# Kernel tuning notes

Measured on AMD Instinct MI355X. Metric: run time of the kernel, lower is better.

## Reference

```python
import jax, jax.numpy as jnp
import numpy as np

N = 50000
E = 1600000
D_IN = 512
EPS = 1e-5


def setup_inputs() -> dict:
    key = jax.random.key(0)
    ks = jax.random.split(key, 20)
    p = lambda k, shape: jax.random.normal(k, shape, dtype=jnp.float32) * 0.05
    return {
        "x": jax.random.normal(ks[0], (N, D_IN), dtype=jnp.float32),
        "edge_index": jax.random.randint(ks[1], (2, E), 0, N),
        "edge_weight": jax.random.uniform(ks[2], (E,), dtype=jnp.float32),
        # conv1: ChebConv(512->400) with K=1,2,3 (weight per Chebyshev order)
        "W1a": p(ks[3], (1, D_IN, 400)), "b1a": p(ks[4], (400,)),
        "W1b": p(ks[5], (2, D_IN, 400)), "b1b": p(ks[6], (400,)),
        "W1c": p(ks[7], (3, D_IN, 400)), "b1c": p(ks[8], (400,)),
        "g1": jnp.ones((1200,), jnp.float32), "beta1": jnp.zeros((1200,), jnp.float32),
        # conv2: ChebConv(1200->100) with K=1,2,3
        "W2a": p(ks[9], (1, 1200, 100)), "b2a": p(ks[10], (100,)),
        "W2b": p(ks[11], (2, 1200, 100)), "b2b": p(ks[12], (100,)),
        "W2c": p(ks[13], (3, 1200, 100)), "b2c": p(ks[14], (100,)),
        "g2": jnp.ones((300,), jnp.float32), "beta2": jnp.zeros((300,), jnp.float32),
        "Wl": p(ks[15], (300, 10)), "bl": p(ks[16], (10,)),
    }


def _cheb(x, row, col, norm, W, b):
    """PyG ChebConv forward: out = sum_k T_k(L_hat) x @ W[k] + b.
    L_hat (sym norm, lambda_max=2) = -D^{-1/2} A D^{-1/2}, zero diagonal,
    applied as scatter: (L_hat h)[col] += norm_e * h[row]."""
    K = W.shape[0]
    n = x.shape[0]
    prop = lambda h: jax.ops.segment_sum(norm[:, None] * h[row], col, num_segments=n)
    out = x @ W[0]
    Tx_prev, Tx = x, None
    if K >= 2:
        Tx = prop(x)
        out = out + Tx @ W[1]
    for k in range(2, K):
        Tx_new = 2.0 * prop(Tx) - Tx_prev
        out = out + Tx_new @ W[k]
        Tx_prev, Tx = Tx, Tx_new
    return out + b


def _bn(h, g, beta):
    # BatchNorm over nodes (training-mode batch statistics, biased var)
    mu = h.mean(axis=0)
    var = h.var(axis=0)
    return (h - mu) * jax.lax.rsqrt(var + EPS) * g + beta


def reference(x, edge_index, edge_weight, W1a, b1a, W1b, b1b, W1c, b1c, g1, beta1,
              W2a, b2a, W2b, b2b, W2c, b2c, g2, beta2, Wl, bl):
    row, col = edge_index[0], edge_index[1]
    deg = jax.ops.segment_sum(edge_weight, row, num_segments=x.shape[0])
    safe = jnp.where(deg > 0, deg, 1.0)
    dis = jnp.where(deg > 0, jax.lax.rsqrt(safe), 0.0)  # deg^{-1/2}, inf -> 0
    norm = -dis[row] * edge_weight * dis[col]  # scaled-Laplacian edge weights

    h = jnp.concatenate([
        _cheb(x, row, col, norm, W1a, b1a),
        _cheb(x, row, col, norm, W1b, b1b),
        _cheb(x, row, col, norm, W1c, b1c)], axis=1)  # [N, 1200]
    h = jax.nn.relu(_bn(h, g1, beta1))

    h = jnp.concatenate([
        _cheb(h, row, col, norm, W2a, b2a),
        _cheb(h, row, col, norm, W2b, b2b),
        _cheb(h, row, col, norm, W2c, b2c)], axis=1)  # [N, 300]
    h = _bn(h, g2, beta2)

    logits = h @ Wl + bl  # [N, 10]
    return jax.nn.log_softmax(logits, axis=1)
```

## Files before the change

kernel.cpp:

```cpp
#include <hip/hip_runtime.h>
#include <math.h>

#define EPSB 1e-5f

typedef __attribute__((ext_vector_type(8))) short short8;
typedef __attribute__((ext_vector_type(4))) float floatx4;
typedef __attribute__((ext_vector_type(2))) float floatx2;

__device__ inline float bf2f(unsigned short h) {
  union { unsigned int u; float f; } v; v.u = ((unsigned int)h) << 16; return v.f;
}
__device__ inline unsigned short f2bf(float f) {
  union { float f; unsigned int u; } v; v.f = f;
  unsigned int r = v.u + 0x7fffu + ((v.u >> 16) & 1u);
  return (unsigned short)(r >> 16);
}

__device__ __forceinline__ void gl2lds16(const unsigned short* g, unsigned short* l) {
  __builtin_amdgcn_global_load_lds(
      (const __attribute__((address_space(1))) unsigned int*)g,
      (__attribute__((address_space(3))) unsigned int*)l, 16, 0, 0);
}

__device__ __forceinline__ void pk4(floatx2* a, uint4 g, floatx2 wv) {
  unsigned int u[4] = {g.x, g.y, g.z, g.w};
#pragma unroll
  for (int j = 0; j < 4; j++) {
    union { unsigned int q; float f; } lo, hi;
    lo.q = u[j] << 16;
    hi.q = u[j] & 0xffff0000u;
    floatx2 v; v[0] = lo.f; v[1] = hi.f;
    asm("v_pk_fma_f32 %0, %1, %2, %0" : "+v"(a[j]) : "v"(v), "v"(wv));
  }
}


__global__ void degcnt_kernel(const int* __restrict__ row, const int* __restrict__ col,
                              const float* __restrict__ ew,
                              float* __restrict__ deg, int* __restrict__ cnt, int E) {
  int e = blockIdx.x * blockDim.x + threadIdx.x;
  if (e < E) {
    atomicAdd(&deg[row[e]], ew[e]);
    atomicAdd(&cnt[col[e]], 1);
  }
}

__global__ void dis_kernel(float* deg, int n) {
  int i = blockIdx.x * blockDim.x + threadIdx.x;
  if (i < n) { float d = deg[i]; deg[i] = d > 0.f ? rsqrtf(d) : 0.f; }
}

__global__ __launch_bounds__(1024) void scan1_kernel(const int* __restrict__ cnt,
                                                     int* __restrict__ off,
                                                     int* __restrict__ bsum, int n) {
  __shared__ int buf[1024];
  int tid = threadIdx.x;
  int idx = blockIdx.x * 1024 + tid;
  int v = (idx < n) ? cnt[idx] : 0;
  buf[tid] = v;
  __syncthreads();
  for (int s = 1; s < 1024; s <<= 1) {
    int t = (tid >= s) ? buf[tid - s] : 0;
    __syncthreads();
    if (tid >= s) buf[tid] += t;
    __syncthreads();
  }
  if (idx < n) off[idx] = buf[tid] - v;
  if (tid == 1023) bsum[blockIdx.x] = buf[1023];
}

__global__ void scan2_kernel(int* __restrict__ bsum, int* __restrict__ off,
                             int nb, int n) {
  if (threadIdx.x == 0 && blockIdx.x == 0) {
    int run = 0;
    for (int k = 0; k < nb; k++) { int t = bsum[k]; bsum[k] = run; run += t; }
    off[n] = run;
  }
}

__global__ void scan3_kernel(int* __restrict__ off, const int* __restrict__ bsum, int n) {
  int i = blockIdx.x * blockDim.x + threadIdx.x;
  if (i < n) off[i] += bsum[i >> 10];
}

__global__ void copy_kernel(const int* __restrict__ src, int* __restrict__ dst, int n) {
  int i = blockIdx.x * blockDim.x + threadIdx.x;
  if (i < n) dst[i] = src[i];
}

__global__ void fill_kernel(const int* __restrict__ row, const int* __restrict__ col,
                            const float* __restrict__ ew, const float* __restrict__ dis,
                            int* __restrict__ wptr, int2* __restrict__ ePack, int E) {
  int e = blockIdx.x * blockDim.x + threadIdx.x;
  if (e < E) {
    int r = row[e], c = col[e];
    int p = atomicAdd(&wptr[c], 1);
    float nv = -dis[r] * ew[e] * dis[c];
    ePack[p] = make_int2(r, __float_as_int(nv));
  }
}


__global__ void cast_x_kernel(const float* __restrict__ x, unsigned short* __restrict__ xb,
                              int N) {
  int idx = blockIdx.x * blockDim.x + threadIdx.x;
  if (idx >= N * 128) return;
  int row = idx >> 7, c4 = idx & 127;
  float4 v = *reinterpret_cast<const float4*>(x + (size_t)row * 512 + c4 * 4);
  union { unsigned int u[2]; } p;
  p.u[0] = (unsigned int)f2bf(v.x) | ((unsigned int)f2bf(v.y) << 16);
  p.u[1] = (unsigned int)f2bf(v.z) | ((unsigned int)f2bf(v.w) << 16);
  *reinterpret_cast<uint2*>(xb + (size_t)row * 1536 + c4 * 4) = make_uint2(p.u[0], p.u[1]);
}

__global__ void wprep_kernel(const float* __restrict__ W, unsigned short* __restrict__ Bt,
                             int Ktot, int Nout, int ldBt, int rowOff) {
  int idx = blockIdx.x * blockDim.x + threadIdx.x;
  if (idx >= Ktot * Nout) return;
  int k = idx / Nout, n = idx - k * Nout;
  Bt[(size_t)(rowOff + n) * ldBt + k] = f2bf(W[idx]);
}

__global__ void padzero_kernel(unsigned short* __restrict__ h, int N) {
  int i = blockIdx.x * blockDim.x + threadIdx.x;
  if (i >= N * 2) return;
  *reinterpret_cast<uint4*>(h + (size_t)(i >> 1) * 1216 + 1200 + (i & 1) * 8) =
      make_uint4(0, 0, 0, 0);
}

__global__ void bcat_kernel(const float* __restrict__ a, const float* __restrict__ b,
                            const float* __restrict__ c, float* __restrict__ dst, int seg) {
  int i = blockIdx.x * blockDim.x + threadIdx.x;
  if (i >= 3 * seg) return;
  float v;
  if (i < seg) v = a[i];
  else if (i < 2 * seg) v = b[i - seg];
  else v = c[i - 2 * seg];
  dst[i] = v;
}

__global__ __launch_bounds__(256) void prop_chunk_kernel(
    unsigned short* __restrict__ base, int ld,
    int srcCol, int dstCol, int subCol,
    const int* __restrict__ off, const int2* __restrict__ ePack,
    float scale, int N) {
  int chunk = blockIdx.x & 7;
  int g = blockIdx.x >> 3;
  int tid = threadIdx.x;
  int slot = (tid >> 3) & 3;
  int c8 = tid & 7;
  int v = g * 8 + (tid >> 5);
  bool valid = v < N;
  int vv = valid ? v : N - 1;
  int co = chunk * 64 + c8 * 8;
  const unsigned short* src = base + srcCol + co;
  int s = off[vv], e = off[vv + 1];
  int len = e - s;
  int s0 = s + (len * slot >> 2);
  int e0 = s + (len * (slot + 1) >> 2);
  floatx2 a2[4] = {}, b2[4] = {};
  int i = s0;
  for (; i + 3 < e0; i += 4) {
    int2 p0 = ePack[i];
    int2 p1 = ePack[i + 1];
    int2 p2 = ePack[i + 2];
    int2 p3 = ePack[i + 3];
    uint4 g0 = *reinterpret_cast<const uint4*>(src + (size_t)p0.x * ld);
    uint4 g1 = *reinterpret_cast<const uint4*>(src + (size_t)p1.x * ld);
    uint4 g2 = *reinterpret_cast<const uint4*>(src + (size_t)p2.x * ld);
    uint4 g3 = *reinterpret_cast<const uint4*>(src + (size_t)p3.x * ld);
    floatx2 w0; w0[0] = w0[1] = __int_as_float(p0.y);
    floatx2 w1; w1[0] = w1[1] = __int_as_float(p1.y);
    floatx2 w2; w2[0] = w2[1] = __int_as_float(p2.y);
    floatx2 w3; w3[0] = w3[1] = __int_as_float(p3.y);
    pk4(a2, g0, w0);
    pk4(b2, g1, w1);
    pk4(a2, g2, w2);
    pk4(b2, g3, w3);
  }
  for (; i < e0; i++) {
    int2 p = ePack[i];
    uint4 gg = *reinterpret_cast<const uint4*>(src + (size_t)p.x * ld);
    floatx2 wv; wv[0] = wv[1] = __int_as_float(p.y);
    pk4(a2, gg, wv);
  }
  float a[8];
#pragma unroll
  for (int j = 0; j < 4; j++) {
    a[2 * j]     = a2[j][0] + b2[j][0];
    a[2 * j + 1] = a2[j][1] + b2[j][1];
  }
#pragma unroll
  for (int j = 0; j < 8; j++) {
    a[j] += __shfl_xor(a[j], 8);
    a[j] += __shfl_xor(a[j], 16);
  }
  if (slot != 0 || !valid) return;
  if (subCol >= 0) {
    uint4 sv = *reinterpret_cast<const uint4*>(base + subCol + co + (size_t)v * ld);
    a[0] = scale * a[0] - bf2f((unsigned short)(sv.x & 0xffff));
    a[1] = scale * a[1] - bf2f((unsigned short)(sv.x >> 16));
    a[2] = scale * a[2] - bf2f((unsigned short)(sv.y & 0xffff));
    a[3] = scale * a[3] - bf2f((unsigned short)(sv.y >> 16));
    a[4] = scale * a[4] - bf2f((unsigned short)(sv.z & 0xffff));
    a[5] = scale * a[5] - bf2f((unsigned short)(sv.z >> 16));
    a[6] = scale * a[6] - bf2f((unsigned short)(sv.w & 0xffff));
    a[7] = scale * a[7] - bf2f((unsigned short)(sv.w >> 16));
  }
  uint4 o;
  o.x = (unsigned int)f2bf(a[0]) | ((unsigned int)f2bf(a[1]) << 16);
  o.y = (unsigned int)f2bf(a[2]) | ((unsigned int)f2bf(a[3]) << 16);
  o.z = (unsigned int)f2bf(a[4]) | ((unsigned int)f2bf(a[5]) << 16);
  o.w = (unsigned int)f2bf(a[6]) | ((unsigned int)f2bf(a[7]) << 16);
  *reinterpret_cast<uint4*>(base + dstCol + co + (size_t)v * ld) = o;
}

__global__ void prop_z_kernel(const unsigned short* __restrict__ Zcat,
                              const int* __restrict__ off, const int2* __restrict__ ePack,
                              float* __restrict__ h2f, unsigned short* __restrict__ U1) {
  int v = blockIdx.x;
  int f8 = threadIdx.x;
  if (f8 >= 38) return;
  int s = off[v], e = off[v + 1];
  floatx2 a2[4] = {}, b2[4] = {};
  int i = s;
  for (; i + 3 < e; i += 4) {
    int2 p0 = ePack[i];
    int2 p1 = ePack[i + 1];
    int2 p2 = ePack[i + 2];
    int2 p3 = ePack[i + 3];
    uint4 g0 = *reinterpret_cast<const uint4*>(Zcat + (size_t)p0.x * 304 + f8 * 8);
    uint4 g1 = *reinterpret_cast<const uint4*>(Zcat + (size_t)p1.x * 304 + f8 * 8);
    uint4 g2 = *reinterpret_cast<const uint4*>(Zcat + (size_t)p2.x * 304 + f8 * 8);
    uint4 g3 = *reinterpret_cast<const uint4*>(Zcat + (size_t)p3.x * 304 + f8 * 8);
    floatx2 w0; w0[0] = w0[1] = __int_as_float(p0.y);
    floatx2 w1; w1[0] = w1[1] = __int_as_float(p1.y);
    floatx2 w2; w2[0] = w2[1] = __int_as_float(p2.y);
    floatx2 w3; w3[0] = w3[1] = __int_as_float(p3.y);
    pk4(a2, g0, w0);
    pk4(b2, g1, w1);
    pk4(a2, g2, w2);
    pk4(b2, g3, w3);
  }
  for (; i < e; i++) {
    int2 p = ePack[i];
    uint4 raw = *reinterpret_cast<const uint4*>(Zcat + (size_t)p.x * 304 + f8 * 8);
    floatx2 wv; wv[0] = wv[1] = __int_as_float(p.y);
    pk4(a2, raw, wv);
  }
  float a[8];
#pragma unroll
  for (int j = 0; j < 4; j++) {
    a[2 * j]     = a2[j][0] + b2[j][0];
    a[2 * j + 1] = a2[j][1] + b2[j][1];
  }
  if (f8 < 25) {
    float* p = h2f + (size_t)v * 300 + 100 + f8 * 8;
#pragma unroll
    for (int j = 0; j < 8; j++) p[j] += a[j];
  } else {
    uint4 o;
    o.x = (unsigned int)f2bf(a[0]) | ((unsigned int)f2bf(a[1]) << 16);
    o.y = (unsigned int)f2bf(a[2]) | ((unsigned int)f2bf(a[3]) << 16);
    o.z = (unsigned int)f2bf(a[4]) | ((unsigned int)f2bf(a[5]) << 16);
    o.w = (unsigned int)f2bf(a[6]) | ((unsigned int)f2bf(a[7]) << 16);
    *reinterpret_cast<uint4*>(U1 + (size_t)v * 104 + (f8 - 25) * 8) = o;
  }
}

__global__ void prop_u_kernel(const unsigned short* __restrict__ U1,
                              const int* __restrict__ off, const int2* __restrict__ ePack,
                              const unsigned short* __restrict__ Zcat,
                              float* __restrict__ h2f) {
  int v = blockIdx.x;
  int f8 = threadIdx.x;
  if (f8 >= 13) return;
  int s = off[v], e = off[v + 1];
  floatx2 a2[4] = {}, b2[4] = {};
  int i = s;
  for (; i + 3 < e; i += 4) {
    int2 p0 = ePack[i];
    int2 p1 = ePack[i + 1];
    int2 p2 = ePack[i + 2];
    int2 p3 = ePack[i + 3];
    uint4 g0 = *reinterpret_cast<const uint4*>(U1 + (size_t)p0.x * 104 + f8 * 8);
    uint4 g1 = *reinterpret_cast<const uint4*>(U1 + (size_t)p1.x * 104 + f8 * 8);
    uint4 g2 = *reinterpret_cast<const uint4*>(U1 + (size_t)p2.x * 104 + f8 * 8);
    uint4 g3 = *reinterpret_cast<const uint4*>(U1 + (size_t)p3.x * 104 + f8 * 8);
    floatx2 w0; w0[0] = w0[1] = __int_as_float(p0.y);
    floatx2 w1; w1[0] = w1[1] = __int_as_float(p1.y);
    floatx2 w2; w2[0] = w2[1] = __int_as_float(p2.y);
    floatx2 w3; w3[0] = w3[1] = __int_as_float(p3.y);
    pk4(a2, g0, w0);
    pk4(b2, g1, w1);
    pk4(a2, g2, w2);
    pk4(b2, g3, w3);
  }
  for (; i < e; i++) {
    int2 p = ePack[i];
    uint4 raw = *reinterpret_cast<const uint4*>(U1 + (size_t)p.x * 104 + f8 * 8);
    floatx2 wv; wv[0] = wv[1] = __int_as_float(p.y);
    pk4(a2, raw, wv);
  }
  float a[8];
#pragma unroll
  for (int j = 0; j < 4; j++) {
    a[2 * j]     = a2[j][0] + b2[j][0];
    a[2 * j + 1] = a2[j][1] + b2[j][1];
  }
  const unsigned short* z2 = Zcat + (size_t)v * 304 + 200;
  float* p = h2f + (size_t)v * 300 + 200;
#pragma unroll
  for (int j = 0; j < 8; j++) {
    int c = f8 * 8 + j;
    if (c < 100) p[c] += 2.f * a[j] - bf2f(z2[c]);
  }
}


__global__ __launch_bounds__(256) void gemm_l1_kernel(
    const unsigned short* __restrict__ A,
    const unsigned short* __restrict__ Bt,
    int M, const float* __restrict__ bias,
    unsigned short* __restrict__ Cb) {
  __shared__ __align__(16) unsigned short As[128 * 32];
  __shared__ __align__(16) unsigned short Bs[128 * 32];
  const int colTiles = 10;
  int rowTiles = (M + 127) >> 7;
  int L = blockIdx.x;
  int xcd = L & 7, slot = L >> 3;
  int rpx = (rowTiles + 7) >> 3;
  int rloc = slot / colTiles;
  int ct = slot - rloc * colTiles;
  int rt = xcd * rpx + rloc;
  if (rt >= rowTiles) return;
  int row0 = rt << 7, col0 = ct << 7;
  int Kt = (ct < 3) ? 512 : ((ct < 6) ? 1024 : 1536);

  int tid = threadIdx.x;
  int wave = tid >> 6, lane = tid & 63;
  int q = lane >> 4, mn = lane & 15;
  int wr = wave >> 1, wc = wave & 1;
  floatx4 acc[4][4] = {};

  const unsigned short* ga[2];
  const unsigned short* gb[2];
  unsigned short* la[2];
  unsigned short* lb[2];
#pragma unroll
  for (int j = 0; j < 2; j++) {
    int c = j * 256 + tid;
    int r = c >> 2, cw = (c & 3) * 8;
    int gr = row0 + r; if (gr > M - 1) gr = M - 1;
    ga[j] = A + (size_t)gr * 1536 + cw;
    gb[j] = Bt + (size_t)(col0 + r) * 1536 + cw;
    la[j] = &As[(j * 256 + wave * 64) * 8];
    lb[j] = &Bs[(j * 256 + wave * 64) * 8];
  }

  for (int k0 = 0; k0 < Kt; k0 += 32) {
#pragma unroll
    for (int j = 0; j < 2; j++) {
      gl2lds16(ga[j] + k0, la[j]);
      gl2lds16(gb[j] + k0, lb[j]);
    }
    __syncthreads();
    short8 af[4], bf[4];
#pragma unroll
    for (int i = 0; i < 4; i++) {
      af[i] = *reinterpret_cast<const short8*>(&As[(wr * 64 + i * 16 + mn) * 32 + q * 8]);
      bf[i] = *reinterpret_cast<const short8*>(&Bs[(wc * 64 + i * 16 + mn) * 32 + q * 8]);
    }
#pragma unroll
    for (int mi = 0; mi < 4; mi++)
#pragma unroll
      for (int ni = 0; ni < 4; ni++)
        acc[mi][ni] = __builtin_amdgcn_mfma_f32_16x16x32_bf16(af[mi], bf[ni], acc[mi][ni], 0, 0, 0);
    __syncthreads();
  }

#pragma unroll
  for (int mi = 0; mi < 4; mi++) {
#pragma unroll
    for (int ni = 0; ni < 4; ni++) {
      int gcol = col0 + wc * 64 + ni * 16 + mn;
      if (gcol >= 1200) continue;
      float b = bias[gcol];
#pragma unroll
      for (int r = 0; r < 4; r++) {
        int grow = row0 + wr * 64 + mi * 16 + q * 4 + r;
        if (grow >= M) continue;
        Cb[(size_t)grow * 1216 + gcol] = f2bf(acc[mi][ni][r] + b);
      }
    }
  }
}

__global__ __launch_bounds__(256) void gemm_l2_kernel(
    const unsigned short* __restrict__ A,
    const unsigned short* __restrict__ Bt,
    int M, const float* __restrict__ bias,
    unsigned short* __restrict__ Cb, float* __restrict__ Cf) {
  __shared__ __align__(16) unsigned short As[128 * 32];
  __shared__ __align__(16) unsigned short Bs[128 * 32];
  const int colTiles = 5;
  int rowTiles = (M + 127) >> 7;
  int L = blockIdx.x;
  int xcd = L & 7, slot = L >> 3;
  int rpx = (rowTiles + 7) >> 3;
  int rloc = slot / colTiles;
  int ct = slot - rloc * colTiles;
  int rt = xcd * rpx + rloc;
  if (rt >= rowTiles) return;
  int row0 = rt << 7, col0 = ct << 7;

  int tid = threadIdx.x;
  int wave = tid >> 6, lane = tid & 63;
  int q = lane >> 4, mn = lane & 15;
  int wr = wave >> 1, wc = wave & 1;
  floatx4 acc[4][4] = {};

  const unsigned short* ga[2];
  const unsigned short* gb[2];
  unsigned short* la[2];
  unsigned short* lb[2];
#pragma unroll
  for (int j = 0; j < 2; j++) {
    int c = j * 256 + tid;
    int r = c >> 2, cw = (c & 3) * 8;
    int gr = row0 + r; if (gr > M - 1) gr = M - 1;
    ga[j] = A + (size_t)gr * 1216 + cw;
    int gn = col0 + r; if (gn > 607) gn = 607;
    gb[j] = Bt + (size_t)gn * 1216 + cw;
    la[j] = &As[(j * 256 + wave * 64) * 8];
    lb[j] = &Bs[(j * 256 + wave * 64) * 8];
  }

  for (int k0 = 0; k0 < 1216; k0 += 32) {
#pragma unroll
    for (int j = 0; j < 2; j++) {
      gl2lds16(ga[j] + k0, la[j]);
      gl2lds16(gb[j] + k0, lb[j]);
    }
    __syncthreads();
    short8 af[4], bf[4];
#pragma unroll
    for (int i = 0; i < 4; i++) {
      af[i] = *reinterpret_cast<const short8*>(&As[(wr * 64 + i * 16 + mn) * 32 + q * 8]);
      bf[i] = *reinterpret_cast<const short8*>(&Bs[(wc * 64 + i * 16 + mn) * 32 + q * 8]);
    }
#pragma unroll
    for (int mi = 0; mi < 4; mi++)
#pragma unroll
      for (int ni = 0; ni < 4; ni++)
        acc[mi][ni] = __builtin_amdgcn_mfma_f32_16x16x32_bf16(af[mi], bf[ni], acc[mi][ni], 0, 0, 0);
    __syncthreads();
  }

#pragma unroll
  for (int mi = 0; mi < 4; mi++) {
#pragma unroll
    for (int ni = 0; ni < 4; ni++) {
      int gcol = col0 + wc * 64 + ni * 16 + mn;
      if (gcol < 300) {
        float b = bias[gcol];
#pragma unroll
        for (int r = 0; r < 4; r++) {
          int grow = row0 + wr * 64 + mi * 16 + q * 4 + r;
          if (grow >= M) continue;
          Cf[(size_t)grow * 300 + gcol] = acc[mi][ni][r] + b;
        }
      } else if (gcol >= 304 && gcol < 608) {
#pragma unroll
        for (int r = 0; r < 4; r++) {
          int grow = row0 + wr * 64 + mi * 16 + q * 4 + r;
          if (grow >= M) continue;
          Cb[(size_t)grow * 304 + (gcol - 304)] = f2bf(acc[mi][ni][r]);
        }
      }
    }
  }
}

__global__ void bn_stats_bf16_kernel(const unsigned short* __restrict__ h, int ld, int C,
                                     int N, float* __restrict__ sums) {
  int c = blockIdx.x * blockDim.x + threadIdx.x;
  if (c >= C) return;
  int r0 = blockIdx.y * 256;
  int r1 = min(N, r0 + 256);
  float s = 0.f, s2 = 0.f;
  for (int r = r0; r < r1; r++) {
    float v = bf2f(h[(size_t)r * ld + c]);
    s += v; s2 += v * v;
  }
  atomicAdd(&sums[c], s);
  atomicAdd(&sums[C + c], s2);
}

__global__ void scsh_kernel(const float* __restrict__ sums, const float* __restrict__ g,
                            const float* __restrict__ beta, float invN, int C,
                            float* __restrict__ scSh) {
  int c = blockIdx.x * blockDim.x + threadIdx.x;
  if (c >= C) return;
  float mu = sums[c] * invN;
  float var = sums[C + c] * invN - mu * mu;
  float s = rsqrtf(var + EPSB) * g[c];
  scSh[c] = s;
  scSh[C + c] = beta[c] - mu * s;
}

__global__ void bn_apply_bf16_kernel(unsigned short* __restrict__ h, int ld, int C8, int N,
                                     const float* __restrict__ scSh, int Cfull, int relu) {
  int idx = blockIdx.x * blockDim.x + threadIdx.x;
  if (idx >= N * C8) return;
  int row = idx / C8, c8 = idx - row * C8;
  unsigned short* p = h + (size_t)row * ld + c8 * 8;
  uint4 raw = *reinterpret_cast<uint4*>(p);
  float v[8];
  v[0] = bf2f((unsigned short)(raw.x & 0xffff)); v[1] = bf2f((unsigned short)(raw.x >> 16));
  v[2] = bf2f((unsigned short)(raw.y & 0xffff)); v[3] = bf2f((unsigned short)(raw.y >> 16));
  v[4] = bf2f((unsigned short)(raw.z & 0xffff)); v[5] = bf2f((unsigned short)(raw.z >> 16));
  v[6] = bf2f((unsigned short)(raw.w & 0xffff)); v[7] = bf2f((unsigned short)(raw.w >> 16));
#pragma unroll
  for (int j = 0; j < 8; j++) {
    int c = c8 * 8 + j;
    float o = v[j] * scSh[c] + scSh[Cfull + c];
    if (relu) o = fmaxf(o, 0.f);
    v[j] = o;
  }
  uint4 o;
  o.x = (unsigned int)f2bf(v[0]) | ((unsigned int)f2bf(v[1]) << 16);
  o.y = (unsigned int)f2bf(v[2]) | ((unsigned int)f2bf(v[3]) << 16);
  o.z = (unsigned int)f2bf(v[4]) | ((unsigned int)f2bf(v[5]) << 16);
  o.w = (unsigned int)f2bf(v[6]) | ((unsigned int)f2bf(v[7]) << 16);
  *reinterpret_cast<uint4*>(p) = o;
}

__global__ void bn_stats_kernel(const float* __restrict__ h, int C, int N,
                                float* __restrict__ sums) {
  int c = blockIdx.x * blockDim.x + threadIdx.x;
  if (c >= C) return;
  int r0 = blockIdx.y * 256;
  int r1 = min(N, r0 + 256);
  float s = 0.f, s2 = 0.f;
  for (int r = r0; r < r1; r++) {
    float v = h[(size_t)r * C + c];
    s += v; s2 += v * v;
  }
  atomicAdd(&sums[c], s);
  atomicAdd(&sums[C + c], s2);
}

__global__ void bn_apply_kernel(float* __restrict__ h, int C, int N,
                                const float* __restrict__ sums, const float* __restrict__ g,
                                const float* __restrict__ beta, float invN, int relu) {
  int C4 = C >> 2;
  int c4 = blockIdx.x * blockDim.x + threadIdx.x;
  if (c4 >= C4) return;
  float sc[4], sh[4];
#pragma unroll
  for (int j = 0; j < 4; j++) {
    int c = c4 * 4 + j;
    float mu = sums[c] * invN;
    float var = sums[C + c] * invN - mu * mu;
    float s = rsqrtf(var + EPSB) * g[c];
    sc[j] = s; sh[j] = beta[c] - mu * s;
  }
  int r0 = blockIdx.y * 256, r1 = min(N, r0 + 256);
  for (int r = r0; r < r1; r++) {
    float4* p = reinterpret_cast<float4*>(h + (size_t)r * C) + c4;
    float4 v = *p;
    v.x = v.x * sc[0] + sh[0]; v.y = v.y * sc[1] + sh[1];
    v.z = v.z * sc[2] + sh[2]; v.w = v.w * sc[3] + sh[3];
    if (relu) {
      v.x = fmaxf(v.x, 0.f); v.y = fmaxf(v.y, 0.f);
      v.z = fmaxf(v.z, 0.f); v.w = fmaxf(v.w, 0.f);
    }
    *p = v;
  }
}


__global__ __launch_bounds__(256) void final_bn_kernel(const float* __restrict__ h2,
                                                       const float* __restrict__ scSh,
                                                       const float* __restrict__ Wl,
                                                       const float* __restrict__ bl,
                                                       float* __restrict__ out, int N) {
  __shared__ float Ws[3000];
  __shared__ float S[600];
  for (int i = threadIdx.x; i < 3000; i += 256) Ws[i] = Wl[i];
  for (int i = threadIdx.x; i < 600; i += 256) S[i] = scSh[i];
  __syncthreads();
  int r = blockIdx.x * blockDim.x + threadIdx.x;
  if (r >= N) return;
  float acc[10];
#pragma unroll
  for (int c = 0; c < 10; c++) acc[c] = bl[c];
  const float* hr = h2 + (size_t)r * 300;
  for (int k = 0; k < 300; k++) {
    float x = hr[k] * S[k] + S[300 + k];
#pragma unroll
    for (int c = 0; c < 10; c++) acc[c] += x * Ws[k * 10 + c];
  }
  float mx = acc[0];
#pragma unroll
  for (int c = 1; c < 10; c++) mx = fmaxf(mx, acc[c]);
  float se = 0.f;
#pragma unroll
  for (int c = 0; c < 10; c++) se += expf(acc[c] - mx);
  float lz = mx + logf(se);
#pragma unroll
  for (int c = 0; c < 10; c++) out[(size_t)r * 10 + c] = acc[c] - lz;
}

__global__ __launch_bounds__(256) void final_kernel(const float* __restrict__ h2,
                                                    const float* __restrict__ Wl,
                                                    const float* __restrict__ bl,
                                                    float* __restrict__ out, int N) {
  __shared__ float Ws[3000];
  for (int i = threadIdx.x; i < 3000; i += 256) Ws[i] = Wl[i];
  __syncthreads();
  int r = blockIdx.x * blockDim.x + threadIdx.x;
  if (r >= N) return;
  float acc[10];
#pragma unroll
  for (int c = 0; c < 10; c++) acc[c] = bl[c];
  const float* hr = h2 + (size_t)r * 300;
  for (int k = 0; k < 300; k++) {
    float x = hr[k];
#pragma unroll
    for (int c = 0; c < 10; c++) acc[c] += x * Ws[k * 10 + c];
  }
  float mx = acc[0];
#pragma unroll
  for (int c = 1; c < 10; c++) mx = fmaxf(mx, acc[c]);
  float se = 0.f;
#pragma unroll
  for (int c = 0; c < 10; c++) se += expf(acc[c] - mx);
  float lz = mx + logf(se);
#pragma unroll
  for (int c = 0; c < 10; c++) out[(size_t)r * 10 + c] = acc[c] - lz;
}


__global__ void prop_kernel(const float* __restrict__ src, int srcLd4, int D4,
                            const int* __restrict__ off, const int2* __restrict__ ePack,
                            float* __restrict__ dst, int dstLd4,
                            const float* __restrict__ sub, int subLd4, float scale) {
  int v = blockIdx.x;
  int f4 = threadIdx.x;
  if (f4 >= D4) return;
  int s = off[v], e = off[v + 1];
  float ax = 0.f, ay = 0.f, az = 0.f, aw = 0.f;
  for (int i = s; i < e; i++) {
    int2 p = ePack[i];
    float w = __int_as_float(p.y);
    const float4 hv = *reinterpret_cast<const float4*>(src + ((size_t)p.x * srcLd4 + f4) * 4);
    ax += w * hv.x; ay += w * hv.y; az += w * hv.z; aw += w * hv.w;
  }
  float4 o;
  if (sub) {
    const float4 sv = *reinterpret_cast<const float4*>(sub + ((size_t)v * subLd4 + f4) * 4);
    o.x = scale * ax - sv.x; o.y = scale * ay - sv.y;
    o.z = scale * az - sv.z; o.w = scale * aw - sv.w;
  } else {
    o.x = ax; o.y = ay; o.z = az; o.w = aw;
  }
  *reinterpret_cast<float4*>(dst + ((size_t)v * dstLd4 + f4) * 4) = o;
}

#define BM 64
#define BN 64
#define BK 16

__global__ __launch_bounds__(256) void gemm_kernel(
    const float* __restrict__ A, int lda,
    const float* __restrict__ B, int ldb,
    float* __restrict__ C, int ldc, int c0,
    int M, int Nc, int K,
    const float* __restrict__ bias, int accumulate) {
  __shared__ float As[BK][BM + 4];
  __shared__ float Bs[BK][BN + 4];
  int tid = threadIdx.x;
  int tx = tid & 15, ty = tid >> 4;
  int row0 = blockIdx.y * BM, col0 = blockIdx.x * BN;
  float acc[4][4] = {};
  int aM = tid >> 2;
  int aK = (tid & 3) << 2;
  int bK = tid >> 4;
  int bN = (tid & 15) << 2;
  for (int k0 = 0; k0 < K; k0 += BK) {
    float4 av = make_float4(0.f, 0.f, 0.f, 0.f);
    int ar = row0 + aM;
    if (ar < M && k0 + aK < K)
      av = *reinterpret_cast<const float4*>(A + (size_t)ar * lda + k0 + aK);
    As[aK + 0][aM] = av.x; As[aK + 1][aM] = av.y;
    As[aK + 2][aM] = av.z; As[aK + 3][aM] = av.w;
    float4 bv = make_float4(0.f, 0.f, 0.f, 0.f);
    int bc = col0 + bN;
    if (bc < Nc && k0 + bK < K)
      bv = *reinterpret_cast<const float4*>(B + (size_t)(k0 + bK) * ldb + bc);
    Bs[bK][bN + 0] = bv.x; Bs[bK][bN + 1] = bv.y;
    Bs[bK][bN + 2] = bv.z; Bs[bK][bN + 3] = bv.w;
    __syncthreads();
#pragma unroll
    for (int k = 0; k < BK; k++) {
      float a0 = As[k][ty * 4 + 0], a1 = As[k][ty * 4 + 1];
      float a2 = As[k][ty * 4 + 2], a3 = As[k][ty * 4 + 3];
      float b0 = Bs[k][tx * 4 + 0], b1 = Bs[k][tx * 4 + 1];
      float b2 = Bs[k][tx * 4 + 2], b3 = Bs[k][tx * 4 + 3];
      acc[0][0] += a0 * b0; acc[0][1] += a0 * b1; acc[0][2] += a0 * b2; acc[0][3] += a0 * b3;
      acc[1][0] += a1 * b0; acc[1][1] += a1 * b1; acc[1][2] += a1 * b2; acc[1][3] += a1 * b3;
      acc[2][0] += a2 * b0; acc[2][1] += a2 * b1; acc[2][2] += a2 * b2; acc[2][3] += a2 * b3;
      acc[3][0] += a3 * b0; acc[3][1] += a3 * b1; acc[3][2] += a3 * b2; acc[3][3] += a3 * b3;
    }
    __syncthreads();
  }
#pragma unroll
  for (int i = 0; i < 4; i++) {
    int r = row0 + ty * 4 + i;
    if (r >= M) continue;
#pragma unroll
    for (int j = 0; j < 4; j++) {
      int c = col0 + tx * 4 + j;
      if (c >= Nc) continue;
      float v = acc[i][j];
      if (bias) v += bias[c];
      float* p = C + (size_t)r * ldc + c0 + c;
      if (accumulate) *p += v; else *p = v;
    }
  }
}


static inline int gemm_grid_ct(int M, int colTiles) {
  int rowTiles = (M + 127) >> 7;
  int rpx = (rowTiles + 7) >> 3;
  return 8 * rpx * colTiles;
}

extern "C" void kernel_launch(void* const* d_in, const int* in_sizes, int n_in,
                              void* d_out, int out_size, void* d_ws, size_t ws_size,
                              hipStream_t stream) {
  const float* x   = (const float*)d_in[0];
  const int*   ei  = (const int*)d_in[1];
  const float* ew  = (const float*)d_in[2];
  const float* W1a = (const float*)d_in[3];
  const float* b1a = (const float*)d_in[4];
  const float* W1b = (const float*)d_in[5];
  const float* b1b = (const float*)d_in[6];
  const float* W1c = (const float*)d_in[7];
  const float* b1c = (const float*)d_in[8];
  const float* g1  = (const float*)d_in[9];
  const float* be1 = (const float*)d_in[10];
  const float* W2a = (const float*)d_in[11];
  const float* b2a = (const float*)d_in[12];
  const float* W2b = (const float*)d_in[13];
  const float* b2b = (const float*)d_in[14];
  const float* W2c = (const float*)d_in[15];
  const float* b2c = (const float*)d_in[16];
  const float* g2  = (const float*)d_in[17];
  const float* be2 = (const float*)d_in[18];
  const float* Wl  = (const float*)d_in[19];
  const float* bl  = (const float*)d_in[20];
  float* out = (float*)d_out;

  const int N = in_sizes[0] / 512;
  const int E = in_sizes[1] / 2;
  const int* row = ei;
  const int* col = ei + E;
  (void)n_in; (void)out_size;

  int eb = (E + 255) / 256;
  int nb = (N + 255) / 256;
  int nb1 = (N + 1023) / 1024;

  char* ws = (char*)d_ws;
  size_t o = 0;
  int2*  ePack = (int2*)(ws + o);  o += (size_t)E * 8;
  float* dis   = (float*)(ws + o); o += (size_t)N * 4;
  int*   cnt   = (int*)(ws + o);   o += (size_t)N * 4;
  int*   off   = (int*)(ws + o);   o += (size_t)(N + 4) * 4;
  int*   wptr  = (int*)(ws + o);   o += (size_t)N * 4;
  int*   bsum  = (int*)(ws + o);   o += (size_t)(nb1 + 4) * 4;
  float* sums  = (float*)(ws + o); o += 2400 * 4;
  float* scSh  = (float*)(ws + o); o += 2400 * 4;
  float* bcat1 = (float*)(ws + o); o += 1200 * 4;
  float* bcat2 = (float*)(ws + o); o += 304 * 4;
  o = (o + 255) & ~(size_t)255;
  size_t oCommon = o;

  size_t oA = oCommon;
  unsigned short* BtL1 = (unsigned short*)(ws + oA); oA += (size_t)1280 * 1536 * 2;
  unsigned short* BtL2 = (unsigned short*)(ws + oA); oA += (size_t)640 * 1216 * 2;
  oA = (oA + 255) & ~(size_t)255;
  unsigned short* h1n = (unsigned short*)(ws + oA); oA += (size_t)N * 1216 * 2;
  oA = (oA + 255) & ~(size_t)255;
  float* h2f = (float*)(ws + oA); oA += (size_t)N * 300 * 4;
  oA = (oA + 255) & ~(size_t)255;
  unsigned short* Xcat = (unsigned short*)(ws + oA); oA += (size_t)N * 1536 * 2;
  unsigned short* Zcat = Xcat;
  unsigned short* U1 = Xcat + (size_t)N * 304;

  bool planA = (ws_size >= oA);

  hipMemsetAsync(dis, 0, (size_t)N * 4, stream);
  hipMemsetAsync(cnt, 0, (size_t)N * 4, stream);
  degcnt_kernel<<<eb, 256, 0, stream>>>(row, col, ew, dis, cnt, E);
  dis_kernel<<<nb, 256, 0, stream>>>(dis, N);
  scan1_kernel<<<nb1, 1024, 0, stream>>>(cnt, off, bsum, N);
  scan2_kernel<<<1, 64, 0, stream>>>(bsum, off, nb1, N);
  scan3_kernel<<<nb, 256, 0, stream>>>(off, bsum, N);
  copy_kernel<<<nb, 256, 0, stream>>>(off, wptr, N);
  fill_kernel<<<eb, 256, 0, stream>>>(row, col, ew, dis, wptr, ePack, E);

  if (planA) {
    hipMemsetAsync(BtL1, 0, (size_t)1280 * 1536 * 2, stream);
    hipMemsetAsync(BtL2, 0, (size_t)640 * 1216 * 2, stream);
    wprep_kernel<<<(400 * 512 + 255) / 256, 256, 0, stream>>>(W1a, BtL1, 512, 400, 1536, 0);
    wprep_kernel<<<(400 * 1024 + 255) / 256, 256, 0, stream>>>(W1b, BtL1, 1024, 400, 1536, 400);
    wprep_kernel<<<(400 * 1536 + 255) / 256, 256, 0, stream>>>(W1c, BtL1, 1536, 400, 1536, 800);
    wprep_kernel<<<(100 * 1200 + 255) / 256, 256, 0, stream>>>(W2a, BtL2, 1200, 100, 1216, 0);
    wprep_kernel<<<(100 * 1200 + 255) / 256, 256, 0, stream>>>(W2b, BtL2, 1200, 100, 1216, 100);
    wprep_kernel<<<(100 * 1200 + 255) / 256, 256, 0, stream>>>(W2c, BtL2, 1200, 100, 1216, 200);
    wprep_kernel<<<(100 * 1200 + 255) / 256, 256, 0, stream>>>(W2b + 1200 * 100, BtL2, 1200, 100, 1216, 304);
    wprep_kernel<<<(100 * 1200 + 255) / 256, 256, 0, stream>>>(W2c + 1200 * 100, BtL2, 1200, 100, 1216, 404);
    wprep_kernel<<<(100 * 1200 + 255) / 256, 256, 0, stream>>>(W2c + 2 * 1200 * 100, BtL2, 1200, 100, 1216, 504);
    bcat_kernel<<<(1200 + 255) / 256, 256, 0, stream>>>(b1a, b1b, b1c, bcat1, 400);
    bcat_kernel<<<(300 + 255) / 256, 256, 0, stream>>>(b2a, b2b, b2c, bcat2, 100);
    cast_x_kernel<<<(N * 128 + 255) / 256, 256, 0, stream>>>(x, Xcat, N);
    padzero_kernel<<<(N * 2 + 255) / 256, 256, 0, stream>>>(h1n, N);

    int gridP = ((N + 7) / 8) * 8;
    prop_chunk_kernel<<<gridP, 256, 0, stream>>>(Xcat, 1536, 0, 512, -1,
                                                 off, ePack, 1.f, N);
    prop_chunk_kernel<<<gridP, 256, 0, stream>>>(Xcat, 1536, 512, 1024, 0,
                                                 off, ePack, 2.f, N);

    gemm_l1_kernel<<<gemm_grid_ct(N, 10), 256, 0, stream>>>(Xcat, BtL1, N, bcat1, h1n);

    hipMemsetAsync(sums, 0, 2400 * 4, stream);
    dim3 s1g((1200 + 255) / 256, (N + 255) / 256);
    bn_stats_bf16_kernel<<<s1g, 256, 0, stream>>>(h1n, 1216, 1200, N, sums);
    scsh_kernel<<<(1200 + 255) / 256, 256, 0, stream>>>(sums, g1, be1, 1.f / (float)N, 1200, scSh);
    bn_apply_bf16_kernel<<<((size_t)N * 150 + 255) / 256, 256, 0, stream>>>(
        h1n, 1216, 150, N, scSh, 1200, 1);

    gemm_l2_kernel<<<gemm_grid_ct(N, 5), 256, 0, stream>>>(h1n, BtL2, N, bcat2, Zcat, h2f);

    prop_z_kernel<<<N, 64, 0, stream>>>(Zcat, off, ePack, h2f, U1);
    prop_u_kernel<<<N, 64, 0, stream>>>(U1, off, ePack, Zcat, h2f);

    hipMemsetAsync(sums, 0, 2400 * 4, stream);
    dim3 s2g((300 + 255) / 256, (N + 255) / 256);
    bn_stats_kernel<<<s2g, 256, 0, stream>>>(h2f, 300, N, sums);
    scsh_kernel<<<(300 + 255) / 256, 256, 0, stream>>>(sums, g2, be2, 1.f / (float)N, 300, scSh);
    final_bn_kernel<<<nb, 256, 0, stream>>>(h2f, scSh, Wl, bl, out, N);
    return;
  }

  size_t oB = oCommon;
  float* h2 = (float*)(ws + oB); oB += (size_t)N * 300 * 4;
  oB = (oB + 255) & ~(size_t)255;
  float* h1 = (float*)(ws + oB); oB += (size_t)N * 1200 * 4;
  oB = (oB + 255) & ~(size_t)255;
  size_t avail = (ws_size > oB) ? (ws_size - oB) : 0;
  int C1 = 64;
  { const int opts[4] = {512, 256, 128, 64};
    for (int i = 0; i < 4; i++)
      if ((size_t)2 * N * opts[i] * 4 <= avail) { C1 = opts[i]; break; } }
  int C2 = 100;
  { const int opts[6] = {1200, 600, 400, 300, 200, 100};
    for (int i = 0; i < 6; i++)
      if ((size_t)2 * N * opts[i] * 4 <= avail) { C2 = opts[i]; break; } }
  int maxC = C1 > C2 ? C1 : C2;
  float* S1 = (float*)(ws + oB);
  float* S2 = S1 + (size_t)N * maxC;

  dim3 g1d((400 + BN - 1) / BN, (N + BM - 1) / BM);
  gemm_kernel<<<g1d, 256, 0, stream>>>(x, 512, W1a, 400, h1, 1200, 0,   N, 400, 512, b1a, 0);
  gemm_kernel<<<g1d, 256, 0, stream>>>(x, 512, W1b, 400, h1, 1200, 400, N, 400, 512, b1b, 0);
  gemm_kernel<<<g1d, 256, 0, stream>>>(x, 512, W1c, 400, h1, 1200, 800, N, 400, 512, b1c, 0);
  for (int c = 0; c < 512; c += C1) {
    int D4 = C1 / 4;
    int bt = ((D4 + 63) / 64) * 64;
    prop_kernel<<<N, bt, 0, stream>>>(x + c, 128, D4, off, ePack, S1, D4, nullptr, 0, 1.f);
    gemm_kernel<<<g1d, 256, 0, stream>>>(S1, C1, W1b + (size_t)(512 + c) * 400, 400, h1, 1200, 400, N, 400, C1, nullptr, 1);
    gemm_kernel<<<g1d, 256, 0, stream>>>(S1, C1, W1c + (size_t)(512 + c) * 400, 400, h1, 1200, 800, N, 400, C1, nullptr, 1);
    prop_kernel<<<N, bt, 0, stream>>>(S1, D4, D4, off, ePack, S2, D4, x + c, 128, 2.f);
    gemm_kernel<<<g1d, 256, 0, stream>>>(S2, C1, W1c + (size_t)(2 * 512 + c) * 400, 400, h1, 1200, 800, N, 400, C1, nullptr, 1);
  }

  hipMemsetAsync(sums, 0, 2400 * 4, stream);
  dim3 s1g((1200 + 255) / 256, (N + 255) / 256);
  bn_stats_kernel<<<s1g, 256, 0, stream>>>(h1, 1200, N, sums);
  dim3 a1g((300 + 63) / 64, (N + 255) / 256);
  bn_apply_kernel<<<a1g, 64, 0, stream>>>(h1, 1200, N, sums, g1, be1, 1.f / (float)N, 1);

  dim3 g2d((100 + BN - 1) / BN, (N + BM - 1) / BM);
  gemm_kernel<<<g2d, 256, 0, stream>>>(h1, 1200, W2a, 100, h2, 300, 0,   N, 100, 1200, b2a, 0);
  gemm_kernel<<<g2d, 256, 0, stream>>>(h1, 1200, W2b, 100, h2, 300, 100, N, 100, 1200, b2b, 0);
  gemm_kernel<<<g2d, 256, 0, stream>>>(h1, 1200, W2c, 100, h2, 300, 200, N, 100, 1200, b2c, 0);
  for (int c = 0; c < 1200; c += C2) {
    int D4 = C2 / 4;
    int bt = ((D4 + 63) / 64) * 64;
    prop_kernel<<<N, bt, 0, stream>>>(h1 + c, 300, D4, off, ePack, S1, D4, nullptr, 0, 1.f);
    gemm_kernel<<<g2d, 256, 0, stream>>>(S1, C2, W2b + (size_t)(1200 + c) * 100, 100, h2, 300, 100, N, 100, C2, nullptr, 1);
    gemm_kernel<<<g2d, 256, 0, stream>>>(S1, C2, W2c + (size_t)(1200 + c) * 100, 100, h2, 300, 200, N, 100, C2, nullptr, 1);
    prop_kernel<<<N, bt, 0, stream>>>(S1, D4, D4, off, ePack, S2, D4, h1 + c, 300, 2.f);
    gemm_kernel<<<g2d, 256, 0, stream>>>(S2, C2, W2c + (size_t)(2 * 1200 + c) * 100, 100, h2, 300, 200, N, 100, C2, nullptr, 1);
  }

  hipMemsetAsync(sums, 0, 2400 * 4, stream);
  dim3 s2g((300 + 255) / 256, (N + 255) / 256);
  bn_stats_kernel<<<s2g, 256, 0, stream>>>(h2, 300, N, sums);
  dim3 a2g((75 + 63) / 64, (N + 255) / 256);
  bn_apply_kernel<<<a2g, 64, 0, stream>>>(h2, 300, N, sums, g2, be2, 1.f / (float)N, 0);

  final_kernel<<<nb, 256, 0, stream>>>(h2, Wl, bl, out, N);
}
```

Baseline: 1.681 ms.

## Vectorize prep and BN-stats kernels, pack several nodes per prop block

Cast and weight-prep kernels now write 16-byte packed bf16 vectors. The weight-prep kernel reads eight strided input elements per thread instead of one. The layer-1 BN statistics kernel loads uint4 rows covering 8 channels per thread with smaller row chunks. The layer-2 propagation kernels pack 6 or 19 nodes into each 256-thread block instead of one node per 64-thread block, so fewer lanes sit idle and fewer tiny blocks are launched. The trade-offs are more atomics per thread in BN stats and unbalanced edge counts inside a block.

```diff
diff --git a/kernel.cpp b/kernel.cpp
--- a/kernel.cpp
+++ b/kernel.cpp
@@ -104,21 +104,33 @@
 __global__ void cast_x_kernel(const float* __restrict__ x, unsigned short* __restrict__ xb,
                               int N) {
   int idx = blockIdx.x * blockDim.x + threadIdx.x;
-  if (idx >= N * 128) return;
-  int row = idx >> 7, c4 = idx & 127;
-  float4 v = *reinterpret_cast<const float4*>(x + (size_t)row * 512 + c4 * 4);
-  union { unsigned int u[2]; } p;
-  p.u[0] = (unsigned int)f2bf(v.x) | ((unsigned int)f2bf(v.y) << 16);
-  p.u[1] = (unsigned int)f2bf(v.z) | ((unsigned int)f2bf(v.w) << 16);
-  *reinterpret_cast<uint2*>(xb + (size_t)row * 1536 + c4 * 4) = make_uint2(p.u[0], p.u[1]);
+  if (idx >= N * 64) return;
+  int row = idx >> 6, c8 = idx & 63;
+  float4 v0 = *reinterpret_cast<const float4*>(x + (size_t)row * 512 + c8 * 8);
+  float4 v1 = *reinterpret_cast<const float4*>(x + (size_t)row * 512 + c8 * 8 + 4);
+  uint4 o;
+  o.x = (unsigned int)f2bf(v0.x) | ((unsigned int)f2bf(v0.y) << 16);
+  o.y = (unsigned int)f2bf(v0.z) | ((unsigned int)f2bf(v0.w) << 16);
+  o.z = (unsigned int)f2bf(v1.x) | ((unsigned int)f2bf(v1.y) << 16);
+  o.w = (unsigned int)f2bf(v1.z) | ((unsigned int)f2bf(v1.w) << 16);
+  *reinterpret_cast<uint4*>(xb + (size_t)row * 1536 + c8 * 8) = o;
 }
 
 __global__ void wprep_kernel(const float* __restrict__ W, unsigned short* __restrict__ Bt,
                              int Ktot, int Nout, int ldBt, int rowOff) {
+  int K8 = Ktot >> 3;
   int idx = blockIdx.x * blockDim.x + threadIdx.x;
-  if (idx >= Ktot * Nout) return;
-  int k = idx / Nout, n = idx - k * Nout;
-  Bt[(size_t)(rowOff + n) * ldBt + k] = f2bf(W[idx]);
+  if (idx >= Nout * K8) return;
+  int k8 = idx / Nout, n = idx - k8 * Nout;
+  unsigned short t[8];
+#pragma unroll
+  for (int j = 0; j < 8; j++) t[j] = f2bf(W[(size_t)(k8 * 8 + j) * Nout + n]);
+  uint4 o;
+  o.x = (unsigned int)t[0] | ((unsigned int)t[1] << 16);
+  o.y = (unsigned int)t[2] | ((unsigned int)t[3] << 16);
+  o.z = (unsigned int)t[4] | ((unsigned int)t[5] << 16);
+  o.w = (unsigned int)t[6] | ((unsigned int)t[7] << 16);
+  *reinterpret_cast<uint4*>(Bt + (size_t)(rowOff + n) * ldBt + k8 * 8) = o;
 }
 
 __global__ void padzero_kernel(unsigned short* __restrict__ h, int N) {
@@ -215,12 +227,16 @@
   *reinterpret_cast<uint4*>(base + dstCol + co + (size_t)v * ld) = o;
 }
 
-__global__ void prop_z_kernel(const unsigned short* __restrict__ Zcat,
-                              const int* __restrict__ off, const int2* __restrict__ ePack,
-                              float* __restrict__ h2f, unsigned short* __restrict__ U1) {
-  int v = blockIdx.x;
-  int f8 = threadIdx.x;
-  if (f8 >= 38) return;
+__global__ __launch_bounds__(256) void prop_z_kernel(
+    const unsigned short* __restrict__ Zcat,
+    const int* __restrict__ off, const int2* __restrict__ ePack,
+    float* __restrict__ h2f, unsigned short* __restrict__ U1, int N) {
+  int tid = threadIdx.x;
+  if (tid >= 228) return;
+  int local = tid / 38;
+  int unit = tid - local * 38;
+  int v = blockIdx.x * 6 + local;
+  if (v >= N) return;
   int s = off[v], e = off[v + 1];
   floatx2 a2[4] = {}, b2[4] = {};
   int i = s;
@@ -229,10 +245,10 @@
     int2 p1 = ePack[i + 1];
     int2 p2 = ePack[i + 2];
     int2 p3 = ePack[i + 3];
-    uint4 g0 = *reinterpret_cast<const uint4*>(Zcat + (size_t)p0.x * 304 + f8 * 8);
-    uint4 g1 = *reinterpret_cast<const uint4*>(Zcat + (size_t)p1.x * 304 + f8 * 8);
-    uint4 g2 = *reinterpret_cast<const uint4*>(Zcat + (size_t)p2.x * 304 + f8 * 8);
-    uint4 g3 = *reinterpret_cast<const uint4*>(Zcat + (size_t)p3.x * 304 + f8 * 8);
+    uint4 g0 = *reinterpret_cast<const uint4*>(Zcat + (size_t)p0.x * 304 + unit * 8);
+    uint4 g1 = *reinterpret_cast<const uint4*>(Zcat + (size_t)p1.x * 304 + unit * 8);
+    uint4 g2 = *reinterpret_cast<const uint4*>(Zcat + (size_t)p2.x * 304 + unit * 8);
+    uint4 g3 = *reinterpret_cast<const uint4*>(Zcat + (size_t)p3.x * 304 + unit * 8);
     floatx2 w0; w0[0] = w0[1] = __int_as_float(p0.y);
     floatx2 w1; w1[0] = w1[1] = __int_as_float(p1.y);
     floatx2 w2; w2[0] = w2[1] = __int_as_float(p2.y);
@@ -244,7 +260,7 @@
   }
   for (; i < e; i++) {
     int2 p = ePack[i];
-    uint4 raw = *reinterpret_cast<const uint4*>(Zcat + (size_t)p.x * 304 + f8 * 8);
+    uint4 raw = *reinterpret_cast<const uint4*>(Zcat + (size_t)p.x * 304 + unit * 8);
     floatx2 wv; wv[0] = wv[1] = __int_as_float(p.y);
     pk4(a2, raw, wv);
   }
@@ -254,8 +270,8 @@
     a[2 * j]     = a2[j][0] + b2[j][0];
     a[2 * j + 1] = a2[j][1] + b2[j][1];
   }
-  if (f8 < 25) {
-    float* p = h2f + (size_t)v * 300 + 100 + f8 * 8;
+  if (unit < 25) {
+    float* p = h2f + (size_t)v * 300 + 100 + unit * 8;
 #pragma unroll
     for (int j = 0; j < 8; j++) p[j] += a[j];
   } else {
@@ -264,17 +280,20 @@
     o.y = (unsigned int)f2bf(a[2]) | ((unsigned int)f2bf(a[3]) << 16);
     o.z = (unsigned int)f2bf(a[4]) | ((unsigned int)f2bf(a[5]) << 16);
     o.w = (unsigned int)f2bf(a[6]) | ((unsigned int)f2bf(a[7]) << 16);
-    *reinterpret_cast<uint4*>(U1 + (size_t)v * 104 + (f8 - 25) * 8) = o;
-  }
-}
-
-__global__ void prop_u_kernel(const unsigned short* __restrict__ U1,
-                              const int* __restrict__ off, const int2* __restrict__ ePack,
-                              const unsigned short* __restrict__ Zcat,
-                              float* __restrict__ h2f) {
-  int v = blockIdx.x;
-  int f8 = threadIdx.x;
-  if (f8 >= 13) return;
+    *reinterpret_cast<uint4*>(U1 + (size_t)v * 104 + (unit - 25) * 8) = o;
+  }
+}
+
+__global__ __launch_bounds__(256) void prop_u_kernel(
+    const unsigned short* __restrict__ U1,
+    const int* __restrict__ off, const int2* __restrict__ ePack,
+    const unsigned short* __restrict__ Zcat, float* __restrict__ h2f, int N) {
+  int tid = threadIdx.x;
+  if (tid >= 247) return;
+  int local = tid / 13;
+  int unit = tid - local * 13;
+  int v = blockIdx.x * 19 + local;
+  if (v >= N) return;
   int s = off[v], e = off[v + 1];
   floatx2 a2[4] = {}, b2[4] = {};
   int i = s;
@@ -283,10 +302,10 @@
     int2 p1 = ePack[i + 1];
     int2 p2 = ePack[i + 2];
     int2 p3 = ePack[i + 3];
-    uint4 g0 = *reinterpret_cast<const uint4*>(U1 + (size_t)p0.x * 104 + f8 * 8);
-    uint4 g1 = *reinterpret_cast<const uint4*>(U1 + (size_t)p1.x * 104 + f8 * 8);
-    uint4 g2 = *reinterpret_cast<const uint4*>(U1 + (size_t)p2.x * 104 + f8 * 8);
-    uint4 g3 = *reinterpret_cast<const uint4*>(U1 + (size_t)p3.x * 104 + f8 * 8);
+    uint4 g0 = *reinterpret_cast<const uint4*>(U1 + (size_t)p0.x * 104 + unit * 8);
+    uint4 g1 = *reinterpret_cast<const uint4*>(U1 + (size_t)p1.x * 104 + unit * 8);
+    uint4 g2 = *reinterpret_cast<const uint4*>(U1 + (size_t)p2.x * 104 + unit * 8);
+    uint4 g3 = *reinterpret_cast<const uint4*>(U1 + (size_t)p3.x * 104 + unit * 8);
     floatx2 w0; w0[0] = w0[1] = __int_as_float(p0.y);
     floatx2 w1; w1[0] = w1[1] = __int_as_float(p1.y);
     floatx2 w2; w2[0] = w2[1] = __int_as_float(p2.y);
@@ -298,7 +317,7 @@
   }
   for (; i < e; i++) {
     int2 p = ePack[i];
-    uint4 raw = *reinterpret_cast<const uint4*>(U1 + (size_t)p.x * 104 + f8 * 8);
+    uint4 raw = *reinterpret_cast<const uint4*>(U1 + (size_t)p.x * 104 + unit * 8);
     floatx2 wv; wv[0] = wv[1] = __int_as_float(p.y);
     pk4(a2, raw, wv);
   }
@@ -312,7 +331,7 @@
   float* p = h2f + (size_t)v * 300 + 200;
 #pragma unroll
   for (int j = 0; j < 8; j++) {
-    int c = f8 * 8 + j;
+    int c = unit * 8 + j;
     if (c < 100) p[c] += 2.f * a[j] - bf2f(z2[c]);
   }
 }
@@ -482,19 +501,29 @@
   }
 }
 
-__global__ void bn_stats_bf16_kernel(const unsigned short* __restrict__ h, int ld, int C,
-                                     int N, float* __restrict__ sums) {
-  int c = blockIdx.x * blockDim.x + threadIdx.x;
-  if (c >= C) return;
-  int r0 = blockIdx.y * 256;
-  int r1 = min(N, r0 + 256);
-  float s = 0.f, s2 = 0.f;
+__global__ void bn_stats_bf16_kernel(const unsigned short* __restrict__ h, int N,
+                                     float* __restrict__ sums) {
+  int c8 = blockIdx.x * blockDim.x + threadIdx.x;
+  if (c8 >= 150) return;
+  int r0 = blockIdx.y * 128;
+  int r1 = min(N, r0 + 128);
+  float s[8] = {}, s2[8] = {};
   for (int r = r0; r < r1; r++) {
-    float v = bf2f(h[(size_t)r * ld + c]);
-    s += v; s2 += v * v;
-  }
-  atomicAdd(&sums[c], s);
-  atomicAdd(&sums[C + c], s2);
+    uint4 raw = *reinterpret_cast<const uint4*>(h + (size_t)r * 1216 + c8 * 8);
+    float v[8];
+    v[0] = bf2f((unsigned short)(raw.x & 0xffff)); v[1] = bf2f((unsigned short)(raw.x >> 16));
+    v[2] = bf2f((unsigned short)(raw.y & 0xffff)); v[3] = bf2f((unsigned short)(raw.y >> 16));
+    v[4] = bf2f((unsigned short)(raw.z & 0xffff)); v[5] = bf2f((unsigned short)(raw.z >> 16));
+    v[6] = bf2f((unsigned short)(raw.w & 0xffff)); v[7] = bf2f((unsigned short)(raw.w >> 16));
+#pragma unroll
+    for (int j = 0; j < 8; j++) { s[j] += v[j]; s2[j] += v[j] * v[j]; }
+  }
+#pragma unroll
+  for (int j = 0; j < 8; j++) {
+    int c = c8 * 8 + j;
+    atomicAdd(&sums[c], s[j]);
+    atomicAdd(&sums[1200 + c], s2[j]);
+  }
 }
 
 __global__ void scsh_kernel(const float* __restrict__ sums, const float* __restrict__ g,
@@ -817,18 +846,18 @@
   if (planA) {
     hipMemsetAsync(BtL1, 0, (size_t)1280 * 1536 * 2, stream);
     hipMemsetAsync(BtL2, 0, (size_t)640 * 1216 * 2, stream);
-    wprep_kernel<<<(400 * 512 + 255) / 256, 256, 0, stream>>>(W1a, BtL1, 512, 400, 1536, 0);
-    wprep_kernel<<<(400 * 1024 + 255) / 256, 256, 0, stream>>>(W1b, BtL1, 1024, 400, 1536, 400);
-    wprep_kernel<<<(400 * 1536 + 255) / 256, 256, 0, stream>>>(W1c, BtL1, 1536, 400, 1536, 800);
-    wprep_kernel<<<(100 * 1200 + 255) / 256, 256, 0, stream>>>(W2a, BtL2, 1200, 100, 1216, 0);
-    wprep_kernel<<<(100 * 1200 + 255) / 256, 256, 0, stream>>>(W2b, BtL2, 1200, 100, 1216, 100);
-    wprep_kernel<<<(100 * 1200 + 255) / 256, 256, 0, stream>>>(W2c, BtL2, 1200, 100, 1216, 200);
-    wprep_kernel<<<(100 * 1200 + 255) / 256, 256, 0, stream>>>(W2b + 1200 * 100, BtL2, 1200, 100, 1216, 304);
-    wprep_kernel<<<(100 * 1200 + 255) / 256, 256, 0, stream>>>(W2c + 1200 * 100, BtL2, 1200, 100, 1216, 404);
-    wprep_kernel<<<(100 * 1200 + 255) / 256, 256, 0, stream>>>(W2c + 2 * 1200 * 100, BtL2, 1200, 100, 1216, 504);
+    wprep_kernel<<<(400 * 64 + 255) / 256, 256, 0, stream>>>(W1a, BtL1, 512, 400, 1536, 0);
+    wprep_kernel<<<(400 * 128 + 255) / 256, 256, 0, stream>>>(W1b, BtL1, 1024, 400, 1536, 400);
+    wprep_kernel<<<(400 * 192 + 255) / 256, 256, 0, stream>>>(W1c, BtL1, 1536, 400, 1536, 800);
+    wprep_kernel<<<(100 * 150 + 255) / 256, 256, 0, stream>>>(W2a, BtL2, 1200, 100, 1216, 0);
+    wprep_kernel<<<(100 * 150 + 255) / 256, 256, 0, stream>>>(W2b, BtL2, 1200, 100, 1216, 100);
+    wprep_kernel<<<(100 * 150 + 255) / 256, 256, 0, stream>>>(W2c, BtL2, 1200, 100, 1216, 200);
+    wprep_kernel<<<(100 * 150 + 255) / 256, 256, 0, stream>>>(W2b + 1200 * 100, BtL2, 1200, 100, 1216, 304);
+    wprep_kernel<<<(100 * 150 + 255) / 256, 256, 0, stream>>>(W2c + 1200 * 100, BtL2, 1200, 100, 1216, 404);
+    wprep_kernel<<<(100 * 150 + 255) / 256, 256, 0, stream>>>(W2c + 2 * 1200 * 100, BtL2, 1200, 100, 1216, 504);
     bcat_kernel<<<(1200 + 255) / 256, 256, 0, stream>>>(b1a, b1b, b1c, bcat1, 400);
     bcat_kernel<<<(300 + 255) / 256, 256, 0, stream>>>(b2a, b2b, b2c, bcat2, 100);
-    cast_x_kernel<<<(N * 128 + 255) / 256, 256, 0, stream>>>(x, Xcat, N);
+    cast_x_kernel<<<(N * 64 + 255) / 256, 256, 0, stream>>>(x, Xcat, N);
     padzero_kernel<<<(N * 2 + 255) / 256, 256, 0, stream>>>(h1n, N);
 
     int gridP = ((N + 7) / 8) * 8;
@@ -840,16 +869,16 @@
     gemm_l1_kernel<<<gemm_grid_ct(N, 10), 256, 0, stream>>>(Xcat, BtL1, N, bcat1, h1n);
 
     hipMemsetAsync(sums, 0, 2400 * 4, stream);
-    dim3 s1g((1200 + 255) / 256, (N + 255) / 256);
-    bn_stats_bf16_kernel<<<s1g, 256, 0, stream>>>(h1n, 1216, 1200, N, sums);
+    dim3 s1g((150 + 63) / 64, (N + 127) / 128);
+    bn_stats_bf16_kernel<<<s1g, 64, 0, stream>>>(h1n, N, sums);
     scsh_kernel<<<(1200 + 255) / 256, 256, 0, stream>>>(sums, g1, be1, 1.f / (float)N, 1200, scSh);
     bn_apply_bf16_kernel<<<((size_t)N * 150 + 255) / 256, 256, 0, stream>>>(
         h1n, 1216, 150, N, scSh, 1200, 1);
 
     gemm_l2_kernel<<<gemm_grid_ct(N, 5), 256, 0, stream>>>(h1n, BtL2, N, bcat2, Zcat, h2f);
 
-    prop_z_kernel<<<N, 64, 0, stream>>>(Zcat, off, ePack, h2f, U1);
-    prop_u_kernel<<<N, 64, 0, stream>>>(U1, off, ePack, Zcat, h2f);
+    prop_z_kernel<<<(N + 5) / 6, 256, 0, stream>>>(Zcat, off, ePack, h2f, U1, N);
+    prop_u_kernel<<<(N + 18) / 19, 256, 0, stream>>>(U1, off, ePack, Zcat, h2f, N);
 
     hipMemsetAsync(sums, 0, 2400 * 4, stream);
     dim3 s2g((300 + 255) / 256, (N + 255) / 256);
```

Measured after the change: 1.721 ms. 1.02x slower.
